# Kernel optimization log

Hardware: AMD Instinct MI355X
Metric: run time of the kernel (lower is better)

## Reference

```python
import jax, jax.numpy as jnp
import numpy as np

H = 128      # hidden_dim
HEADS = 4
HD = H // HEADS
B, S, D, A, I = 64, 512, 64, 3, 13


def layernorm(x, g, b, eps=1e-5):
    m = x.mean(-1, keepdims=True)
    v = ((x - m) ** 2).mean(-1, keepdims=True)
    return g * (x - m) / jnp.sqrt(v + eps) + b


def setup_inputs() -> dict:
    key = jax.random.key(0)
    ks = jax.random.split(key, 12)
    rn = lambda k, shp, s=0.05: jax.random.normal(k, shp, jnp.float32) * s
    return {
        "x": jax.random.normal(ks[0], (B, S, D), jnp.float32),
        "info": jax.random.normal(ks[1], (B, I), jnp.float32),
        "W_cell": rn(ks[2], (4 * H, D + H)), "b_cell": jnp.zeros(4 * H, jnp.float32),
        "Wqkv": rn(ks[3], (3 * H, H)), "bqkv": jnp.zeros(3 * H, jnp.float32),
        "Wo": rn(ks[4], (H, H)), "bo": jnp.zeros(H, jnp.float32),
        "ln_g": jnp.ones(H, jnp.float32), "ln_b": jnp.zeros(H, jnp.float32),
        "Wa1": rn(ks[5], (128, H + I)), "ba1": jnp.zeros(128, jnp.float32),
        "lna_g": jnp.ones(128, jnp.float32), "lna_b": jnp.zeros(128, jnp.float32),
        "Wa2": rn(ks[6], (A, 128)), "ba2": jnp.zeros(A, jnp.float32),
        "Wc1": rn(ks[7], (128, H + I)), "bc1": jnp.zeros(128, jnp.float32),
        "lnc_g": jnp.ones(128, jnp.float32), "lnc_b": jnp.zeros(128, jnp.float32),
        "Wc2": rn(ks[8], (1, 128)), "bc2": jnp.zeros(1, jnp.float32),
    }


def reference(x, info, W_cell, b_cell, Wqkv, bqkv, Wo, bo, ln_g, ln_b,
              Wa1, ba1, lna_g, lna_b, Wa2, ba2, Wc1, bc1, lnc_g, lnc_b, Wc2, bc2):
    Bx, Sx, _ = x.shape
    h0 = jnp.zeros((Bx, H), x.dtype)
    c0 = jnp.zeros((Bx, H), x.dtype)
    n0 = jnp.ones((Bx, H), x.dtype)

    def step(carry, xt):
        h, c, n = carry
        gates = jnp.concatenate([xt, h], -1) @ W_cell.T + b_cell
        i, f, o, z = jnp.split(gates, 4, axis=-1)
        i = jnp.exp(jnp.clip(i, -5.0, 5.0))
        f = jnp.exp(jnp.clip(f, -5.0, 5.0))
        c = jnp.clip(f * c + i * jnp.tanh(z), -1e6, 1e6)
        n = jnp.clip(f * n + i, 1e-6, 1e6)
        h = jnp.nan_to_num(jax.nn.sigmoid(o) * (c / n), nan=0.0, posinf=0.0, neginf=0.0)
        return (h, c, n), h

    _, hs = jax.lax.scan(step, (h0, c0, n0), jnp.swapaxes(x, 0, 1))  # (S,B,H)
    seq_h = jnp.swapaxes(hs, 0, 1)  # (B,S,H)

    # MultiheadAttention (self-attn, batch_first, shared in_proj)
    qkv = seq_h @ Wqkv.T + bqkv
    q, k, v = jnp.split(qkv, 3, -1)
    split_heads = lambda t: t.reshape(Bx, Sx, HEADS, HD).transpose(0, 2, 1, 3)
    q, k, v = split_heads(q), split_heads(k), split_heads(v)
    scores = jnp.einsum('bhqd,bhkd->bhqk', q, k) / np.sqrt(HD).astype(np.float32)
    attn = jax.nn.softmax(scores, axis=-1)
    av = jnp.einsum('bhqk,bhkd->bhqd', attn, v).transpose(0, 2, 1, 3).reshape(Bx, Sx, H)
    attn_out = av @ Wo.T + bo
    context = layernorm(seq_h + attn_out, ln_g, ln_b).mean(axis=1)  # (B,H)

    comb = jnp.concatenate([context, info], -1)  # (B, H+I)
    action_probs = jax.nn.softmax(
        jax.nn.relu(layernorm(comb @ Wa1.T + ba1, lna_g, lna_b)) @ Wa2.T + ba2, axis=-1)
    value = jax.nn.relu(layernorm(comb @ Wc1.T + bc1, lnc_g, lnc_b)) @ Wc2.T + bc2
    return (action_probs, value)
```

## Files before the change

kernel.cpp:

```cpp
#include <hip/hip_runtime.h>

typedef unsigned short ushort_t;
typedef unsigned int uint_t;

__device__ __forceinline__ float bflo(uint_t u){ union{uint_t i;float f;}v; v.i=u<<16; return v.f; }
__device__ __forceinline__ float bfhi(uint_t u){ union{uint_t i;float f;}v; v.i=u&0xffff0000u; return v.f; }
__device__ __forceinline__ float bfu(ushort_t u){ union{uint_t i;float f;}v; v.i=((uint_t)u)<<16; return v.f; }
__device__ __forceinline__ ushort_t f2b(float f){
  union{float f;uint_t i;}v; v.f=f;
  uint_t r = v.i + 0x7fffu + ((v.i>>16)&1u);
  return (ushort_t)(r>>16);
}
__device__ __forceinline__ void ld8bf(const ushort_t* p, float* w){
  uint4 u = *(const uint4*)p;
  w[0]=bflo(u.x); w[1]=bfhi(u.x); w[2]=bflo(u.y); w[3]=bfhi(u.y);
  w[4]=bflo(u.z); w[5]=bfhi(u.z); w[6]=bflo(u.w); w[7]=bfhi(u.w);
}
__device__ __forceinline__ void cvt8(uint4 u, float* d){
  d[0]=bflo(u.x); d[1]=bfhi(u.x); d[2]=bflo(u.y); d[3]=bfhi(u.y);
  d[4]=bflo(u.z); d[5]=bfhi(u.z); d[6]=bflo(u.w); d[7]=bfhi(u.w);
}
__device__ __forceinline__ float ldin(const void* p, size_t i, int isbf){
  return isbf ? bfu(((const ushort_t*)p)[i]) : ((const float*)p)[i];
}
__device__ __forceinline__ float rlane(float v, int l){
  return __uint_as_float(__builtin_amdgcn_readlane(__float_as_uint(v), l));
}

#define DOT128(acc, Wv, Bv) { float s0_=0.f,s1_=0.f,s2_=0.f,s3_=0.f; \
  _Pragma("unroll") \
  for (int k_=0;k_<128;k_+=4){ float4 h4_ = *(const float4*)&(Bv)[k_]; \
    s0_ += (Wv)[k_]*h4_.x; s1_ += (Wv)[k_+1]*h4_.y; \
    s2_ += (Wv)[k_+2]*h4_.z; s3_ += (Wv)[k_+3]*h4_.w; } \
  acc += (s0_+s1_)+(s2_+s3_); }
#define DOT64A(acc, Wv, Bv) { float s0_=0.f,s1_=0.f,s2_=0.f,s3_=0.f; \
  _Pragma("unroll") \
  for (int k_=0;k_<64;k_+=4){ float4 h4_ = *(const float4*)&(Bv)[k_]; \
    s0_ += (Wv)[k_]*h4_.x; s1_ += (Wv)[k_+1]*h4_.y; \
    s2_ += (Wv)[k_+2]*h4_.z; s3_ += (Wv)[k_+3]*h4_.w; } \
  acc += (s0_+s1_)+(s2_+s3_); }

typedef __attribute__((ext_vector_type(8))) short bf16x8;
typedef __attribute__((ext_vector_type(8))) _Float16 f16x8;
typedef __attribute__((ext_vector_type(4))) float f32x4;
__device__ __forceinline__ bf16x8 bcast8(uint4 u){ return __builtin_bit_cast(bf16x8, u); }
__device__ __forceinline__ f16x8  hcast8(uint4 u){ return __builtin_bit_cast(f16x8, u); }
__device__ __forceinline__ bf16x8 cvt8bf(const float* p){
  float4 a = *(const float4*)p; float4 b = *(const float4*)(p+4);
  uint4 u;
  u.x = (uint_t)f2b(a.x) | ((uint_t)f2b(a.y)<<16);
  u.y = (uint_t)f2b(a.z) | ((uint_t)f2b(a.w)<<16);
  u.z = (uint_t)f2b(b.x) | ((uint_t)f2b(b.y)<<16);
  u.w = (uint_t)f2b(b.z) | ((uint_t)f2b(b.w)<<16);
  return bcast8(u);
}
__device__ __forceinline__ void cvt8hl(const float* p, bf16x8* hi, bf16x8* lo){
  float v[8];
  *(float4*)&v[0] = *(const float4*)p;
  *(float4*)&v[4] = *(const float4*)(p+4);
  ushort_t h[8], l[8];
  #pragma unroll
  for (int j=0;j<8;++j){ h[j] = f2b(v[j]); l[j] = f2b(v[j] - bfu(h[j])); }
  uint4 uh = { (uint_t)h[0]|((uint_t)h[1]<<16), (uint_t)h[2]|((uint_t)h[3]<<16),
               (uint_t)h[4]|((uint_t)h[5]<<16), (uint_t)h[6]|((uint_t)h[7]<<16) };
  uint4 ul = { (uint_t)l[0]|((uint_t)l[1]<<16), (uint_t)l[2]|((uint_t)l[3]<<16),
               (uint_t)l[4]|((uint_t)l[5]<<16), (uint_t)l[6]|((uint_t)l[7]<<16) };
  *hi = bcast8(uh); *lo = bcast8(ul);
}
__device__ __forceinline__ ushort_t f2h(float f){
  _Float16 h = (_Float16)f;
  return __builtin_bit_cast(ushort_t, h);
}
__device__ __forceinline__ float h2f(ushort_t u){
  _Float16 h = __builtin_bit_cast(_Float16, u);
  return (float)h;
}

__global__ void k_detect(const uint_t* __restrict__ lng_raw, int* __restrict__ flag){
  if (threadIdx.x == 0) *flag = (lng_raw[0] == 0x3F803F80u) ? 1 : 0;
}

__global__ __launch_bounds__(256) void k_cvtw(const float* __restrict__ Wq,
    const float* __restrict__ Wo, const float* __restrict__ Wc,
    ushort_t* __restrict__ wqb, ushort_t* __restrict__ wob,
    ushort_t* __restrict__ wxh, ushort_t* __restrict__ wxl,
    ushort_t* __restrict__ whf, ushort_t* __restrict__ whl,
    const int* __restrict__ flag){
  if (*flag == 1) return;
  int i = blockIdx.x*256 + threadIdx.x;
  if (i < 12288){
    float4 f = ((const float4*)Wq)[i];
    uint2 u = { (uint_t)f2b(f.x) | ((uint_t)f2b(f.y)<<16),
                (uint_t)f2b(f.z) | ((uint_t)f2b(f.w)<<16) };
    ((uint2*)wqb)[i] = u;
  } else if (i < 16384){
    int k = i - 12288;
    float4 f = ((const float4*)Wo)[k];
    uint2 u = { (uint_t)f2b(f.x) | ((uint_t)f2b(f.y)<<16),
                (uint_t)f2b(f.z) | ((uint_t)f2b(f.w)<<16) };
    ((uint2*)wob)[k] = u;
  } else if (i < 24576){
    int k = i - 16384;
    int j = k >> 4, kq = (k & 15)*4;
    float4 f = *(const float4*)(Wc + (size_t)j*192 + kq);
    ushort_t h0=f2b(f.x), h1=f2b(f.y), h2=f2b(f.z), h3=f2b(f.w);
    ushort_t l0=f2b(f.x-bfu(h0)), l1=f2b(f.y-bfu(h1));
    ushort_t l2=f2b(f.z-bfu(h2)), l3=f2b(f.w-bfu(h3));
    ((uint2*)(wxh + (size_t)j*64 + kq))[0] = { (uint_t)h0|((uint_t)h1<<16), (uint_t)h2|((uint_t)h3<<16) };
    ((uint2*)(wxl + (size_t)j*64 + kq))[0] = { (uint_t)l0|((uint_t)l1<<16), (uint_t)l2|((uint_t)l3<<16) };
  } else if (i < 32768){
    int k2 = i - 24576;
    int jp = k2 >> 4, kc = (k2 & 15)*8;
    int wvp = jp >> 6, g = (jp >> 4) & 3, l = jp & 15;
    int jorig = 128*g + 16*wvp + l;
    const float* src = Wc + (size_t)jorig*192 + 64 + kc;
    ushort_t hh[8], ll[8];
    #pragma unroll
    for (int q=0;q<8;++q){
      hh[q] = f2h(src[q]);
      ll[q] = f2h(src[q] - h2f(hh[q]));
    }
    uint4 uh = { (uint_t)hh[0]|((uint_t)hh[1]<<16), (uint_t)hh[2]|((uint_t)hh[3]<<16),
                 (uint_t)hh[4]|((uint_t)hh[5]<<16), (uint_t)hh[6]|((uint_t)hh[7]<<16) };
    uint4 ul = { (uint_t)ll[0]|((uint_t)ll[1]<<16), (uint_t)ll[2]|((uint_t)ll[3]<<16),
                 (uint_t)ll[4]|((uint_t)ll[5]<<16), (uint_t)ll[6]|((uint_t)ll[7]<<16) };
    *(uint4*)(whf + (size_t)jp*136 + kc) = uh;
    *(uint4*)(whl + (size_t)jp*128 + kc) = ul;
  }
}

__global__ __launch_bounds__(256) void k_gx_bf(const void* __restrict__ x,
    const void* __restrict__ Wc, const void* __restrict__ bc,
    float* __restrict__ gx, const int* __restrict__ flag){
  if (*flag == 0) return;
  __shared__ float xs[2048];
  int row0 = blockIdx.x*32, t = threadIdx.x;
  {
    uint4 u = ((const uint4*)((const ushort_t*)x + (size_t)row0*64))[t];
    cvt8(u, &xs[t*8]);
  }
  __syncthreads();
  for (int pass=0; pass<2; ++pass){
    int j = t + pass*256;
    float w[64];
    const ushort_t* wr = (const ushort_t*)Wc + (size_t)j*192;
    #pragma unroll
    for (int q=0;q<8;q++) ld8bf(wr + 8*q, &w[8*q]);
    float bj = bfu(((const ushort_t*)bc)[j]);
    for (int s=0;s<32;++s){
      float acc = bj;
      DOT64A(acc, w, &xs[s*64]);
      gx[(size_t)(row0+s)*512 + j] = acc;
    }
  }
}

__global__ __launch_bounds__(256) void k_gx_f32(const float* __restrict__ x,
    const float* __restrict__ bc,
    const ushort_t* __restrict__ wxh, const ushort_t* __restrict__ wxl,
    float* __restrict__ gx, const int* __restrict__ flag){
  if (*flag == 1) return;
  int t = threadIdx.x, lane = t & 63, wave = t >> 6;
  int l16 = lane & 15, quad = lane >> 4;
  int rowb = blockIdx.x*64 + wave*16;
  const float* xp = x + (size_t)(rowb + l16)*64;
  bf16x8 xh0, xl0, xh1, xl1;
  cvt8hl(xp + quad*8,      &xh0, &xl0);
  cvt8hl(xp + 32 + quad*8, &xh1, &xl1);
  int r0 = rowb + quad*4;
  for (int ct=0; ct<32; ++ct){
    int j = ct*16 + l16;
    const ushort_t* bh = wxh + (size_t)j*64 + quad*8;
    const ushort_t* bl = wxl + (size_t)j*64 + quad*8;
    bf16x8 wh0 = bcast8(*(const uint4*)(bh));
    bf16x8 wh1 = bcast8(*(const uint4*)(bh + 32));
    bf16x8 wl0 = bcast8(*(const uint4*)(bl));
    bf16x8 wl1 = bcast8(*(const uint4*)(bl + 32));
    f32x4 acc = {0.f,0.f,0.f,0.f};
    acc = __builtin_amdgcn_mfma_f32_16x16x32_bf16(xh0, wh0, acc, 0,0,0);
    acc = __builtin_amdgcn_mfma_f32_16x16x32_bf16(xh1, wh1, acc, 0,0,0);
    acc = __builtin_amdgcn_mfma_f32_16x16x32_bf16(xh0, wl0, acc, 0,0,0);
    acc = __builtin_amdgcn_mfma_f32_16x16x32_bf16(xh1, wl1, acc, 0,0,0);
    acc = __builtin_amdgcn_mfma_f32_16x16x32_bf16(xl0, wh0, acc, 0,0,0);
    acc = __builtin_amdgcn_mfma_f32_16x16x32_bf16(xl1, wh1, acc, 0,0,0);
    float bj = bc[j];
    #pragma unroll
    for (int r=0;r<4;++r)
      gx[(size_t)(r0+r)*512 + j] = acc[r] + bj;
  }
}

__global__ __attribute__((amdgpu_flat_work_group_size(512,512), amdgpu_waves_per_eu(2,2)))
void k_rec_hl(const ushort_t* __restrict__ whf,
    const ushort_t* __restrict__ whl,
    const float* __restrict__ gx, float* __restrict__ seq_h,
    const int* __restrict__ flag){
  if (*flag == 1) return;
  int b = blockIdx.x, t = threadIdx.x;
  int lane = t & 63, wv = t >> 6, l16 = lane & 15, quad = lane >> 4;
  __shared__ ushort_t wlds[512*136];
  __shared__ ushort_t hz[2][448];
  {
    const uint4* src = (const uint4*)whf;
    uint4* dst = (uint4*)wlds;
    for (int i=t; i<8704; i+=512) dst[i] = src[i];
  }
  if (t < 448){ hz[0][t] = (ushort_t)0; hz[1][t] = (ushort_t)0; }
  const float* gxb = gx + (size_t)b*512*512;
  const int hidx = 16*wv + l16;
  float g0=0.f,g1=0.f,g2=0.f,g3=0.f;
  float c = 0.f, n = 1.f;
  if (quad == 0){
    g0 = gxb[hidx]; g1 = gxb[128+hidx]; g2 = gxb[256+hidx]; g3 = gxb[384+hidx];
  }
  float* shout = seq_h + (size_t)b*512*128;
  __syncthreads();
  const int c0 = 4*wv, c1 = 4*wv+1, c2 = 4*wv+2, c3 = 4*wv+3;
  const ushort_t* w0 = wlds + (c0*16 + l16)*136 + quad*8;
  const ushort_t* w1 = wlds + (c1*16 + l16)*136 + quad*8;
  const ushort_t* w2 = wlds + (c2*16 + l16)*136 + quad*8;
  const ushort_t* w3 = wlds + (c3*16 + l16)*136 + quad*8;
  const ushort_t* p0 = whl + (size_t)(c0*16 + l16)*128 + quad*8;
  const ushort_t* p1 = whl + (size_t)(c1*16 + l16)*128 + quad*8;
  const ushort_t* p2 = whl + (size_t)(c2*16 + l16)*128 + quad*8;
  const ushort_t* p3 = whl + (size_t)(c3*16 + l16)*128 + quad*8;
#define BDECL(T, ptr) uint4 T##0 = *(const uint4*)(ptr), T##1 = *(const uint4*)((ptr)+32), \
  T##2 = *(const uint4*)((ptr)+64), T##3 = *(const uint4*)((ptr)+96);
  BDECL(U0, w0) BDECL(U1, w1) BDECL(U2, w2) BDECL(U3, w3)
  BDECL(V0, p0) BDECL(V1, p1) BDECL(V2, p2) BDECL(V3, p3)
#undef BDECL
#define UPIN(U) asm volatile("" : "+v"(U.x), "+v"(U.y), "+v"(U.z), "+v"(U.w));
  UPIN(U00) UPIN(U01) UPIN(U02) UPIN(U03)
  UPIN(U10) UPIN(U11) UPIN(U12) UPIN(U13)
  UPIN(U20) UPIN(U21) UPIN(U22) UPIN(U23)
  UPIN(U30) UPIN(U31) UPIN(U32) UPIN(U33)
  UPIN(V00) UPIN(V01) UPIN(V02) UPIN(V03)
  UPIN(V10) UPIN(V11) UPIN(V12) UPIN(V13)
  UPIN(V20) UPIN(V21) UPIN(V22) UPIN(V23)
  UPIN(V30) UPIN(V31) UPIN(V32) UPIN(V33)
#undef UPIN
  const int hoff = ((l16 == 0) ? 0 : ((l16 == 1) ? 160 : 320)) + quad*8;
  const ushort_t* hzA = hz[0] + hoff;
  const ushort_t* hzB = hz[1] + hoff;
  for (int ts=0; ts<512; ++ts){
    const ushort_t* src = (ts & 1) ? hzB : hzA;
    ushort_t* dstbuf = (ts & 1) ? hz[0] : hz[1];
    f16x8 A0 = hcast8(*(const uint4*)(src));
    f16x8 A1 = hcast8(*(const uint4*)(src + 32));
    f16x8 A2 = hcast8(*(const uint4*)(src + 64));
    f16x8 A3 = hcast8(*(const uint4*)(src + 96));
    f32x4 s0 = {0.f,0.f,0.f,0.f}, s1 = {0.f,0.f,0.f,0.f};
    f32x4 s2 = {0.f,0.f,0.f,0.f}, s3 = {0.f,0.f,0.f,0.f};
#define TILE(sa, Uf, Vf) \
    sa = __builtin_amdgcn_mfma_f32_16x16x32_f16(A0, hcast8(Uf##0), sa, 0,0,0); \
    sa = __builtin_amdgcn_mfma_f32_16x16x32_f16(A1, hcast8(Uf##1), sa, 0,0,0); \
    sa = __builtin_amdgcn_mfma_f32_16x16x32_f16(A2, hcast8(Uf##2), sa, 0,0,0); \
    sa = __builtin_amdgcn_mfma_f32_16x16x32_f16(A3, hcast8(Uf##3), sa, 0,0,0); \
    sa = __builtin_amdgcn_mfma_f32_16x16x32_f16(A0, hcast8(Vf##0), sa, 0,0,0); \
    sa = __builtin_amdgcn_mfma_f32_16x16x32_f16(A1, hcast8(Vf##1), sa, 0,0,0); \
    sa = __builtin_amdgcn_mfma_f32_16x16x32_f16(A2, hcast8(Vf##2), sa, 0,0,0); \
    sa = __builtin_amdgcn_mfma_f32_16x16x32_f16(A3, hcast8(Vf##3), sa, 0,0,0);
    TILE(s0, U0, V0)
    TILE(s1, U1, V1)
    TILE(s2, U2, V2)
    TILE(s3, U3, V3)
#undef TILE
    if (quad == 0){
      float gi = s0[0] + s0[1] + g0;
      float gf = s1[0] + s1[1] + g1;
      float go = s2[0] + s2[1] + g2;
      float gz = s3[0] + s3[1] + g3;
      if (ts+1 < 512){
        const float* gn = gxb + (size_t)(ts+1)*512;
        g0 = gn[hidx]; g1 = gn[128+hidx]; g2 = gn[256+hidx]; g3 = gn[384+hidx];
      }
      float ii = __expf(fminf(fmaxf(gi,-5.f),5.f));
      float ff = __expf(fminf(fmaxf(gf,-5.f),5.f));
      float e2 = __expf(2.f*gz);
      float zt = 1.f - 2.f/(e2+1.f);
      c = fminf(fmaxf(ff*c + ii*zt, -1e6f), 1e6f);
      n = fminf(fmaxf(ff*n + ii, 1e-6f), 1e6f);
      float oo = 1.f/(1.f+__expf(-go));
      float h = oo*(c/n);
      if (!isfinite(h)) h = 0.f;
      shout[(size_t)ts*128 + hidx] = h;
      ushort_t hhi = f2h(h);
      dstbuf[hidx] = hhi;
      dstbuf[160 + hidx] = f2h(h - h2f(hhi));
    }
    __syncthreads();
  }
}

__global__ __launch_bounds__(1024, 4) void k_rec_bf(const void* __restrict__ Wc,
    const float* __restrict__ gx, float* __restrict__ seq_h,
    const int* __restrict__ flag){
  if (*flag == 0) return;
  int b = blockIdx.x, t = threadIdx.x;
  int lane = t & 63, j = t & 511, half = t >> 9;
  __shared__ float ps[1024];
  __shared__ float hs[128];
  uint_t wu[32];
  {
    const uint4* wp = (const uint4*)((const ushort_t*)Wc + (size_t)j*192 + 64 + 64*half);
    #pragma unroll
    for (int q=0;q<8;q++){ uint4 u = wp[q];
      wu[4*q]=u.x; wu[4*q+1]=u.y; wu[4*q+2]=u.z; wu[4*q+3]=u.w; }
  }
  const float* gxb = gx + (size_t)b*512*512;
  float g0=0.f, g1=0.f;
  if (half==0){ g0 = gxb[j]; g1 = gxb[512 + j]; }
  float hreg = 0.f;
  float c = 0.f, n = 1.f;
  float* shout = seq_h + (size_t)b*512*128;
  for (int ts=0; ts<512; ++ts){
    float a0, a1=0.f, a2=0.f, a3=0.f;
    if (half==0){
      a0 = g0; g0 = g1;
      g1 = (ts+2 < 512) ? gxb[(size_t)(ts+2)*512 + j] : 0.f;
    } else a0 = 0.f;
    #pragma unroll
    for (int kk=0; kk<32; kk+=2){
      float h0v = rlane(hreg, 2*kk),   h1v = rlane(hreg, 2*kk+1);
      float h2v = rlane(hreg, 2*kk+2), h3v = rlane(hreg, 2*kk+3);
      a0 = fmaf(bflo(wu[kk]),   h0v, a0);
      a1 = fmaf(bfhi(wu[kk]),   h1v, a1);
      a2 = fmaf(bflo(wu[kk+1]), h2v, a2);
      a3 = fmaf(bfhi(wu[kk+1]), h3v, a3);
    }
    ps[t] = (a0+a1)+(a2+a3);
    __syncthreads();
    if (t < 128){
      float gi = ps[t]     + ps[512+t];
      float gf = ps[128+t] + ps[640+t];
      float go = ps[256+t] + ps[768+t];
      float gz = ps[384+t] + ps[896+t];
      float ii = __expf(fminf(fmaxf(gi,-5.f),5.f));
      float ff = __expf(fminf(fmaxf(gf,-5.f),5.f));
      float e2 = __expf(2.f*gz);
      float zt = 1.f - 2.f/(e2+1.f);
      c = fminf(fmaxf(ff*c + ii*zt, -1e6f), 1e6f);
      n = fminf(fmaxf(ff*n + ii, 1e-6f), 1e6f);
      float oo = 1.f/(1.f+__expf(-go));
      float h = oo*(c/n);
      if (!isfinite(h)) h = 0.f;
      hs[t] = h;
      shout[(size_t)ts*128 + t] = h;
    }
    __syncthreads();
    hreg = hs[(half<<6) | lane];
  }
}

__global__ __launch_bounds__(512) void k_rec_inl(const void* __restrict__ x,
    const void* __restrict__ Wc, const void* __restrict__ bc,
    float* __restrict__ seq_h, const int* __restrict__ flag){
  int isbf = *flag;
  int b = blockIdx.x, j = threadIdx.x;
  __shared__ float hs[128];
  __shared__ float gs[512];
  __shared__ float xr[4][64];
  float w[128], wx[64];
  if (isbf){
    const ushort_t* wr = (const ushort_t*)Wc + (size_t)j*192;
    #pragma unroll
    for (int q=0;q<8;q++)  ld8bf(wr + 8*q, &wx[8*q]);
    #pragma unroll
    for (int q=0;q<16;q++) ld8bf(wr + 64 + 8*q, &w[8*q]);
  } else {
    const float* wr = (const float*)Wc + (size_t)j*192;
    #pragma unroll
    for (int q=0;q<16;q++){ float4 f=*(const float4*)(wr+4*q);
      wx[4*q]=f.x; wx[4*q+1]=f.y; wx[4*q+2]=f.z; wx[4*q+3]=f.w; }
    #pragma unroll
    for (int q=0;q<32;q++){ float4 f=*(const float4*)(wr+64+4*q);
      w[4*q]=f.x; w[4*q+1]=f.y; w[4*q+2]=f.z; w[4*q+3]=f.w; }
  }
  float bj = ldin(bc, j, isbf);
  float c = 0.f, n = 1.f;
  if (j < 128) hs[j] = 0.f;
  if (j < 128){
    int r = j>>6, k = j&63;
    xr[r][k] = ldin(x, ((size_t)b*512 + r)*64 + k, isbf);
  }
  __syncthreads();
  for (int t=0; t<512; ++t){
    const float* xt = xr[t&3];
    float acc = bj;
    DOT64A(acc, wx, xt);
    DOT128(acc, w, hs);
    gs[j] = acc;
    __syncthreads();
    if (j < 128){
      float gi=gs[j], gf=gs[128+j], go=gs[256+j], gz=gs[384+j];
      float ii = __expf(fminf(fmaxf(gi,-5.f),5.f));
      float ff = __expf(fminf(fmaxf(gf,-5.f),5.f));
      float e2 = __expf(2.f*gz);
      float zt = 1.f - 2.f/(e2+1.f);
      c = fminf(fmaxf(ff*c + ii*zt, -1e6f), 1e6f);
      n = fminf(fmaxf(ff*n + ii, 1e-6f), 1e6f);
      float oo = 1.f/(1.f+__expf(-go));
      float h = oo*(c/n);
      if (!isfinite(h)) h = 0.f;
      hs[j] = h;
      seq_h[((size_t)b*512 + t)*128 + j] = h;
    } else if (j >= 448 && (t+2) < 512){
      int k = j & 63;
      xr[(t+2)&3][k] = ldin(x, ((size_t)b*512 + (t+2))*64 + k, isbf);
    }
    __syncthreads();
  }
}

__global__ __launch_bounds__(256) void k_qkv(const float* __restrict__ seq_h,
    const void* __restrict__ Wq, const void* __restrict__ bq,
    const ushort_t* __restrict__ wqb,
    ushort_t* __restrict__ qkv, const int* __restrict__ flag){
  int isbf = *flag;
  int row0 = blockIdx.x*32, t = threadIdx.x;
  if (isbf){
    __shared__ float hsb[4096];
    {
      const float4* hp = (const float4*)(seq_h + (size_t)row0*128);
      #pragma unroll
      for (int i=t;i<1024;i+=256) ((float4*)hsb)[i] = hp[i];
    }
    __syncthreads();
    for (int pass=0; pass<2; ++pass){
      int j = (pass==0) ? t : 256 + t;
      if (j >= 384) break;
      float w[128];
      const ushort_t* wr = (const ushort_t*)Wq + (size_t)j*128;
      #pragma unroll
      for (int q=0;q<16;q++) ld8bf(wr + 8*q, &w[8*q]);
      float bj = bfu(((const ushort_t*)bq)[j]);
      for (int s=0;s<32;++s){
        float acc = bj;
        DOT128(acc, w, &hsb[s*128]);
        qkv[(size_t)(row0+s)*384 + j] = f2b(acc);
      }
    }
  } else {
    int lane = t & 63, wave = t >> 6, l16 = lane & 15, quad = lane >> 4;
    int rt = wave & 1, chalf = wave >> 1;
    int rowg = row0 + rt*16 + l16;
    const float* hp = seq_h + (size_t)rowg*128 + quad*8;
    bf16x8 A0 = cvt8bf(hp);
    bf16x8 A1 = cvt8bf(hp + 32);
    bf16x8 A2 = cvt8bf(hp + 64);
    bf16x8 A3 = cvt8bf(hp + 96);
    int rbase = row0 + rt*16 + quad*4;
    for (int ci=0; ci<12; ++ci){
      int ct = chalf*12 + ci;
      int col = ct*16 + l16;
      const ushort_t* wb = wqb + (size_t)col*128 + quad*8;
      f32x4 acc = {0.f,0.f,0.f,0.f};
      acc = __builtin_amdgcn_mfma_f32_16x16x32_bf16(A0, bcast8(*(const uint4*)(wb)),      acc, 0,0,0);
      acc = __builtin_amdgcn_mfma_f32_16x16x32_bf16(A1, bcast8(*(const uint4*)(wb + 32)), acc, 0,0,0);
      acc = __builtin_amdgcn_mfma_f32_16x16x32_bf16(A2, bcast8(*(const uint4*)(wb + 64)), acc, 0,0,0);
      acc = __builtin_amdgcn_mfma_f32_16x16x32_bf16(A3, bcast8(*(const uint4*)(wb + 96)), acc, 0,0,0);
      float bj = ((const float*)bq)[col];
      #pragma unroll
      for (int r=0;r<4;++r)
        qkv[(size_t)(rbase+r)*384 + col] = f2b(acc[r] + bj);
    }
  }
}

#define AROW4(OP) OP(0) OP(1) OP(2) OP(3)
__global__ __launch_bounds__(512) void k_attn(const ushort_t* __restrict__ qkv,
    ushort_t* __restrict__ av){
  int b = blockIdx.x >> 2, h = blockIdx.x & 3;
  int t = threadIdx.x, lane = t & 63, wave = t >> 6;
  int l16 = lane & 15, quad = lane >> 4;
  __shared__ ushort_t Vt[32*512];
  __shared__ ushort_t Pl[8*16*64];
  const ushort_t* base = qkv + (size_t)b*512*384 + h*32;
  {
    const ushort_t* vr = base + (size_t)t*384 + 256;
    ushort_t tmp[32];
    *(uint4*)&tmp[0]  = *(const uint4*)(vr);
    *(uint4*)&tmp[8]  = *(const uint4*)(vr+8);
    *(uint4*)&tmp[16] = *(const uint4*)(vr+16);
    *(uint4*)&tmp[24] = *(const uint4*)(vr+24);
    #pragma unroll
    for (int d=0; d<32; ++d) Vt[d*512 + t] = tmp[d];
  }
  __syncthreads();
  ushort_t* Pw = Pl + wave*16*64;
  const float scale = 0.17677669529663687f;
  for (int q4=0; q4<4; ++q4){
    int qt = wave + q4*8;
    bf16x8 qa;
    { uint4 u = *(const uint4*)(base + (size_t)(qt*16 + l16)*384 + quad*8);
      qa = bcast8(u); }
    f32x4 O0 = {0.f,0.f,0.f,0.f}, O1 = {0.f,0.f,0.f,0.f};
    float m0=-1e30f,m1=-1e30f,m2=-1e30f,m3=-1e30f;
    float l0=0.f,l1=0.f,l2=0.f,l3=0.f;
    for (int ch=0; ch<8; ++ch){
      f32x4 S0,S1,S2,S3;
      {
        const ushort_t* kb = base + 128 + quad*8;
        uint4 u0 = *(const uint4*)(kb + (size_t)(ch*64 +  0 + l16)*384);
        uint4 u1 = *(const uint4*)(kb + (size_t)(ch*64 + 16 + l16)*384);
        uint4 u2 = *(const uint4*)(kb + (size_t)(ch*64 + 32 + l16)*384);
        uint4 u3 = *(const uint4*)(kb + (size_t)(ch*64 + 48 + l16)*384);
        f32x4 z = {0.f,0.f,0.f,0.f};
        S0 = __builtin_amdgcn_mfma_f32_16x16x32_bf16(qa, bcast8(u0), z, 0,0,0);
        S1 = __builtin_amdgcn_mfma_f32_16x16x32_bf16(qa, bcast8(u1), z, 0,0,0);
        S2 = __builtin_amdgcn_mfma_f32_16x16x32_bf16(qa, bcast8(u2), z, 0,0,0);
        S3 = __builtin_amdgcn_mfma_f32_16x16x32_bf16(qa, bcast8(u3), z, 0,0,0);
      }
#define CMAX(r) float c##r = fmaxf(fmaxf(S0[r],S1[r]), fmaxf(S2[r],S3[r])) * scale; \
      c##r = fmaxf(c##r, __shfl_xor(c##r,1)); c##r = fmaxf(c##r, __shfl_xor(c##r,2)); \
      c##r = fmaxf(c##r, __shfl_xor(c##r,4)); c##r = fmaxf(c##r, __shfl_xor(c##r,8)); \
      float M##r = fmaxf(m##r, c##r); float al##r = __expf(m##r - M##r); \
      m##r = M##r; O0[r] *= al##r; O1[r] *= al##r; l##r *= al##r;
      AROW4(CMAX)
#undef CMAX
#define PEXP(r) float ps##r; { \
      float p0 = __expf(S0[r]*scale - m##r); \
      float p1 = __expf(S1[r]*scale - m##r); \
      float p2 = __expf(S2[r]*scale - m##r); \
      float p3 = __expf(S3[r]*scale - m##r); \
      ps##r = (p0+p1)+(p2+p3); \
      Pw[(quad*4+(r))*64 +  0 + l16] = f2b(p0); \
      Pw[(quad*4+(r))*64 + 16 + l16] = f2b(p1); \
      Pw[(quad*4+(r))*64 + 32 + l16] = f2b(p2); \
      Pw[(quad*4+(r))*64 + 48 + l16] = f2b(p3); }
      AROW4(PEXP)
#undef PEXP
#define PSUM(r) ps##r += __shfl_xor(ps##r,1); ps##r += __shfl_xor(ps##r,2); \
      ps##r += __shfl_xor(ps##r,4); ps##r += __shfl_xor(ps##r,8); l##r += ps##r;
      AROW4(PSUM)
#undef PSUM
      asm volatile("s_waitcnt lgkmcnt(0)" ::: "memory");
      bf16x8 pa0, pa1;
      { uint4 u = *(const uint4*)&Pw[l16*64 + quad*8];      pa0 = bcast8(u); }
      { uint4 u = *(const uint4*)&Pw[l16*64 + 32 + quad*8]; pa1 = bcast8(u); }
      {
        uint4 v0 = *(const uint4*)&Vt[(l16)*512    + ch*64 + quad*8];
        uint4 v1 = *(const uint4*)&Vt[(l16)*512    + ch*64 + 32 + quad*8];
        uint4 v2 = *(const uint4*)&Vt[(16+l16)*512 + ch*64 + quad*8];
        uint4 v3 = *(const uint4*)&Vt[(16+l16)*512 + ch*64 + 32 + quad*8];
        O0 = __builtin_amdgcn_mfma_f32_16x16x32_bf16(pa0, bcast8(v0), O0, 0,0,0);
        O0 = __builtin_amdgcn_mfma_f32_16x16x32_bf16(pa1, bcast8(v1), O0, 0,0,0);
        O1 = __builtin_amdgcn_mfma_f32_16x16x32_bf16(pa0, bcast8(v2), O1, 0,0,0);
        O1 = __builtin_amdgcn_mfma_f32_16x16x32_bf16(pa1, bcast8(v3), O1, 0,0,0);
      }
    }
#define OST(r) { float iv = 1.f/l##r; int row = qt*16 + quad*4 + (r); \
      ushort_t* op = av + (size_t)(b*512 + row)*128 + h*32; \
      op[l16]      = f2b(O0[r]*iv); \
      op[16 + l16] = f2b(O1[r]*iv); }
    AROW4(OST)
#undef OST
  }
}

__global__ __launch_bounds__(256) void k_ctx(const ushort_t* __restrict__ av,
    const float* __restrict__ seq_h, const void* __restrict__ Wo,
    const void* __restrict__ bo_, const void* __restrict__ lng,
    const void* __restrict__ lnb, const ushort_t* __restrict__ wob,
    float* __restrict__ partial, const int* __restrict__ flag){
  int isbf = *flag;
  __shared__ float rs[4096];
  __shared__ float mrow[32], srow[32];
  __shared__ float halfsum[128];
  int row0 = blockIdx.x*32, t = threadIdx.x;
  int j = t & 127, sh = t >> 7;
  if (isbf){
    __shared__ float avs[4096];
    {
      const uint4* ap = (const uint4*)(av + (size_t)row0*128);
      for (int i=t;i<512;i+=256) cvt8(ap[i], &avs[i*8]);
    }
    __syncthreads();
    float w[128];
    const ushort_t* wr = (const ushort_t*)Wo + (size_t)j*128;
    #pragma unroll
    for (int q=0;q<16;q++) ld8bf(wr + 8*q, &w[8*q]);
    float bj = bfu(((const ushort_t*)bo_)[j]);
    for (int si=0; si<16; ++si){
      int s = sh*16 + si;
      float acc = bj;
      DOT128(acc, w, &avs[s*128]);
      rs[s*128+j] = acc + seq_h[(size_t)(row0+s)*128 + j];
    }
  } else {
    int lane = t & 63, wave = t >> 6, l16 = lane & 15, quad = lane >> 4;
    int rt = wave & 1, chalf = wave >> 1;
    int rowg = row0 + rt*16 + l16;
    const ushort_t* ap = av + (size_t)rowg*128 + quad*8;
    bf16x8 A0 = bcast8(*(const uint4*)(ap));
    bf16x8 A1 = bcast8(*(const uint4*)(ap + 32));
    bf16x8 A2 = bcast8(*(const uint4*)(ap + 64));
    bf16x8 A3 = bcast8(*(const uint4*)(ap + 96));
    int rl0 = rt*16 + quad*4;
    for (int ci=0; ci<4; ++ci){
      int ct = chalf*4 + ci;
      int col = ct*16 + l16;
      const ushort_t* wb = wob + (size_t)col*128 + quad*8;
      f32x4 acc = {0.f,0.f,0.f,0.f};
      acc = __builtin_amdgcn_mfma_f32_16x16x32_bf16(A0, bcast8(*(const uint4*)(wb)),      acc, 0,0,0);
      acc = __builtin_amdgcn_mfma_f32_16x16x32_bf16(A1, bcast8(*(const uint4*)(wb + 32)), acc, 0,0,0);
      acc = __builtin_amdgcn_mfma_f32_16x16x32_bf16(A2, bcast8(*(const uint4*)(wb + 64)), acc, 0,0,0);
      acc = __builtin_amdgcn_mfma_f32_16x16x32_bf16(A3, bcast8(*(const uint4*)(wb + 96)), acc, 0,0,0);
      float bj2 = ((const float*)bo_)[col];
      #pragma unroll
      for (int r=0;r<4;++r){
        int rl = rl0 + r;
        rs[rl*128 + col] = acc[r] + bj2 + seq_h[(size_t)(row0+rl)*128 + col];
      }
    }
  }
  __syncthreads();
  {
    int rr = t>>3, part = t&7;
    float vals[16], sm = 0.f;
    #pragma unroll
    for (int k2=0;k2<16;k2++){ vals[k2] = rs[rr*128 + part + 8*k2]; sm += vals[k2]; }
    sm += __shfl_xor(sm,1); sm += __shfl_xor(sm,2); sm += __shfl_xor(sm,4);
    float mean = sm*(1.f/128.f);
    float vv = 0.f;
    #pragma unroll
    for (int k2=0;k2<16;k2++){ float d = vals[k2]-mean; vv += d*d; }
    vv += __shfl_xor(vv,1); vv += __shfl_xor(vv,2); vv += __shfl_xor(vv,4);
    if (part==0){ mrow[rr]=mean; srow[rr]=rsqrtf(vv*(1.f/128.f)+1e-5f); }
  }
  __syncthreads();
  float g = ldin(lng, j, isbf), bb = ldin(lnb, j, isbf);
  float accs = 0.f;
  for (int si=0; si<16; ++si){
    int s = sh*16 + si;
    accs += g*(rs[s*128+j]-mrow[s])*srow[s] + bb;
  }
  if (sh==0) halfsum[j] = accs;
  __syncthreads();
  if (sh==1){
    int bidx = row0>>9, tile = (row0>>5)&15;
    partial[((size_t)bidx*16 + tile)*128 + j] = halfsum[j] + accs;
  }
}

__global__ __launch_bounds__(128) void k_head(const float* __restrict__ partial,
    const void* __restrict__ info,
    const void* Wa1, const void* ba1, const void* lnag, const void* lnab,
    const void* Wa2, const void* ba2,
    const void* Wc1, const void* bc1, const void* lncg, const void* lncb,
    const void* Wc2, const void* bc2, void* __restrict__ out,
    const int* __restrict__ flag){
  int isbf = *flag;
  int b = blockIdx.x, t = threadIdx.x;
  __shared__ float comb[144];
  __shared__ float red[128];
  __shared__ float uu[128];
  float s = 0.f;
  #pragma unroll
  for (int i=0;i<16;i++) s += partial[((size_t)b*16+i)*128 + t];
  comb[t] = s*(1.f/512.f);
  if (t < 13) comb[128+t] = ldin(info, (size_t)b*13+t, isbf);
  __syncthreads();
  for (int br=0; br<2; ++br){
    const void* W1 = br ? Wc1 : Wa1;
    const void* b1 = br ? bc1 : ba1;
    const void* lg_ = br ? lncg : lnag;
    const void* lb_ = br ? lncb : lnab;
    float a = ldin(b1, t, isbf);
    for (int k=0;k<141;k++) a += ldin(W1, (size_t)t*141+k, isbf)*comb[k];
    red[t] = a; __syncthreads();
    for (int st=64; st>0; st>>=1){ if (t<st) red[t]+=red[t+st]; __syncthreads(); }
    float mean = red[0]*(1.f/128.f);
    __syncthreads();
    float d = a - mean;
    red[t] = d*d; __syncthreads();
    for (int st=64; st>0; st>>=1){ if (t<st) red[t]+=red[t+st]; __syncthreads(); }
    float rstd = rsqrtf(red[0]*(1.f/128.f)+1e-5f);
    __syncthreads();
    float u = ldin(lg_, t, isbf)*d*rstd + ldin(lb_, t, isbf);
    uu[t] = fmaxf(u, 0.f);
    __syncthreads();
    if (br==0){
      if (t < 3){
        float lg2 = ldin(ba2, t, isbf);
        for (int k=0;k<128;k++) lg2 += ldin(Wa2, (size_t)t*128+k, isbf)*uu[k];
        red[t] = lg2;
      }
      __syncthreads();
      if (t==0){
        float mx = fmaxf(red[0], fmaxf(red[1], red[2]));
        float e0=__expf(red[0]-mx), e1=__expf(red[1]-mx), e2=__expf(red[2]-mx);
        float inv = 1.f/(e0+e1+e2);
        if (isbf){
          ushort_t* o = (ushort_t*)out;
          o[b*3+0]=f2b(e0*inv); o[b*3+1]=f2b(e1*inv); o[b*3+2]=f2b(e2*inv);
        } else {
          float* o = (float*)out;
          o[b*3+0]=e0*inv; o[b*3+1]=e1*inv; o[b*3+2]=e2*inv;
        }
      }
      __syncthreads();
    } else {
      if (t==0){
        float v = ldin(bc2, 0, isbf);
        for (int k=0;k<128;k++) v += ldin(Wc2, k, isbf)*uu[k];
        if (isbf) ((ushort_t*)out)[192 + b] = f2b(v);
        else      ((float*)out)[192 + b] = v;
      }
    }
  }
}

extern "C" void kernel_launch(void* const* d_in, const int* in_sizes, int n_in,
                              void* d_out, int out_size, void* d_ws, size_t ws_size,
                              hipStream_t stream){
  const void* x    = d_in[0];
  const void* info = d_in[1];
  const void* Wcell= d_in[2];
  const void* bcell= d_in[3];
  const void* Wqkv = d_in[4];
  const void* bqkv = d_in[5];
  const void* Wo   = d_in[6];
  const void* bo   = d_in[7];
  const void* lng  = d_in[8];
  const void* lnb  = d_in[9];
  const void* Wa1  = d_in[10];
  const void* ba1  = d_in[11];
  const void* lnag = d_in[12];
  const void* lnab = d_in[13];
  const void* Wa2  = d_in[14];
  const void* ba2  = d_in[15];
  const void* Wc1  = d_in[16];
  const void* bc1  = d_in[17];
  const void* lncg = d_in[18];
  const void* lncb = d_in[19];
  const void* Wc2  = d_in[20];
  const void* bc2  = d_in[21];

  char* ws = (char*)d_ws;
  const int bigws = (ws_size >= ((size_t)82<<20)) ? 1 : 0;
  float*    seqh = (float*)   ws;
  float*    gxf  = (float*)   (ws + ((size_t)16<<20));
  ushort_t* qkv  = (ushort_t*)(ws + ((size_t)16<<20));
  ushort_t* av   = (ushort_t*)(ws + ((size_t)40<<20));
  float*    part = (float*)   (ws + ((size_t)48<<20));
  int*      flag = bigws ? (int*)(ws + ((size_t)80<<20))
                         : (int*)(ws + ((size_t)48<<20) + (512<<10));
  ushort_t* wqb  = (ushort_t*)(ws + ((size_t)80<<20) + (1<<20));
  ushort_t* wob  = wqb + 384*128;
  ushort_t* wxh  = wob + 128*128;
  ushort_t* wxl  = wxh + 512*64;
  ushort_t* whf  = wxl + 512*64;
  ushort_t* whl  = whf + 512*136;

  k_detect<<<1, 64, 0, stream>>>((const uint_t*)lng, flag);
  if (bigws){
    k_cvtw  <<< 128, 256, 0, stream>>>((const float*)Wqkv, (const float*)Wo,
                                       (const float*)Wcell, wqb, wob, wxh, wxl, whf, whl, flag);
    k_gx_bf <<<1024, 256, 0, stream>>>(x, Wcell, bcell, gxf, flag);
    k_gx_f32<<< 512, 256, 0, stream>>>((const float*)x, (const float*)bcell,
                                       wxh, wxl, gxf, flag);
    k_rec_bf <<< 64, 1024, 0, stream>>>(Wcell, gxf, seqh, flag);
    k_rec_hl <<< 64,  512, 0, stream>>>(whf, whl, gxf, seqh, flag);
  } else {
    k_rec_inl<<<64, 512, 0, stream>>>(x, Wcell, bcell, seqh, flag);
    k_cvtw  <<< 128, 256, 0, stream>>>((const float*)Wqkv, (const float*)Wo,
                                       (const float*)Wcell, wqb, wob, wxh, wxl, whf, whl, flag);
  }
  k_qkv <<<1024, 256, 0, stream>>>(seqh, Wqkv, bqkv, wqb, qkv, flag);
  k_attn<<< 256, 512, 0, stream>>>(qkv, av);
  k_ctx <<<1024, 256, 0, stream>>>(av, seqh, Wo, bo, lng, lnb, wob, part, flag);
  k_head<<<  64, 128, 0, stream>>>(part, info, Wa1, ba1, lnag, lnab, Wa2, ba2,
                                   Wc1, bc1, lncg, lncb, Wc2, bc2, d_out, flag);
}
```

Measured before the change: 698.2 us.

## Interleave gate layout, prefetch gates four steps ahead, use LDS-only barrier

The input-projection kernel now writes the four gate values of each hidden unit next to each other, so the recurrent kernel can fetch all four with one float4 load. The recurrent loop is unrolled by four, with four rotating float4 registers that prefetch gate inputs four timesteps ahead. __syncthreads is replaced by an explicit lgkmcnt wait plus s_barrier, so the barrier no longer waits for outstanding global loads and the seq_h stores. This is meant to take global-memory latency off the serial 512-step critical path. The risk is that any other reader of gx that still expects the old layout would now get wrong values.

Result: no change. 691.6 us (-1.0%).

```diff
diff --git a/kernel.cpp b/kernel.cpp
--- a/kernel.cpp
+++ b/kernel.cpp
@@ -184,9 +184,10 @@
     acc = __builtin_amdgcn_mfma_f32_16x16x32_bf16(xl0, wh0, acc, 0,0,0);
     acc = __builtin_amdgcn_mfma_f32_16x16x32_bf16(xl1, wh1, acc, 0,0,0);
     float bj = bc[j];
+    int dcol = ((j & 127) << 2) + (j >> 7);
     #pragma unroll
     for (int r=0;r<4;++r)
-      gx[(size_t)(r0+r)*512 + j] = acc[r] + bj;
+      gx[(size_t)(r0+r)*512 + dcol] = acc[r] + bj;
   }
 }
 
@@ -208,10 +209,14 @@
   if (t < 448){ hz[0][t] = (ushort_t)0; hz[1][t] = (ushort_t)0; }
   const float* gxb = gx + (size_t)b*512*512;
   const int hidx = 16*wv + l16;
-  float g0=0.f,g1=0.f,g2=0.f,g3=0.f;
   float c = 0.f, n = 1.f;
+  const float* gxp = gxb + ((size_t)hidx << 2);
+  float4 P0 = {0.f,0.f,0.f,0.f}, P1 = P0, P2 = P0, P3 = P0;
   if (quad == 0){
-    g0 = gxb[hidx]; g1 = gxb[128+hidx]; g2 = gxb[256+hidx]; g3 = gxb[384+hidx];
+    P0 = *(const float4*)(gxp);
+    P1 = *(const float4*)(gxp + 512);
+    P2 = *(const float4*)(gxp + 1024);
+    P3 = *(const float4*)(gxp + 1536);
   }
   float* shout = seq_h + (size_t)b*512*128;
   __syncthreads();
@@ -242,15 +247,6 @@
   const int hoff = ((l16 == 0) ? 0 : ((l16 == 1) ? 160 : 320)) + quad*8;
   const ushort_t* hzA = hz[0] + hoff;
   const ushort_t* hzB = hz[1] + hoff;
-  for (int ts=0; ts<512; ++ts){
-    const ushort_t* src = (ts & 1) ? hzB : hzA;
-    ushort_t* dstbuf = (ts & 1) ? hz[0] : hz[1];
-    f16x8 A0 = hcast8(*(const uint4*)(src));
-    f16x8 A1 = hcast8(*(const uint4*)(src + 32));
-    f16x8 A2 = hcast8(*(const uint4*)(src + 64));
-    f16x8 A3 = hcast8(*(const uint4*)(src + 96));
-    f32x4 s0 = {0.f,0.f,0.f,0.f}, s1 = {0.f,0.f,0.f,0.f};
-    f32x4 s2 = {0.f,0.f,0.f,0.f}, s3 = {0.f,0.f,0.f,0.f};
 #define TILE(sa, Uf, Vf) \
     sa = __builtin_amdgcn_mfma_f32_16x16x32_f16(A0, hcast8(Uf##0), sa, 0,0,0); \
     sa = __builtin_amdgcn_mfma_f32_16x16x32_f16(A1, hcast8(Uf##1), sa, 0,0,0); \
@@ -260,36 +256,54 @@
     sa = __builtin_amdgcn_mfma_f32_16x16x32_f16(A1, hcast8(Vf##1), sa, 0,0,0); \
     sa = __builtin_amdgcn_mfma_f32_16x16x32_f16(A2, hcast8(Vf##2), sa, 0,0,0); \
     sa = __builtin_amdgcn_mfma_f32_16x16x32_f16(A3, hcast8(Vf##3), sa, 0,0,0);
-    TILE(s0, U0, V0)
-    TILE(s1, U1, V1)
-    TILE(s2, U2, V2)
-    TILE(s3, U3, V3)
+#define STEPBODY(TS, PAR, PS) { \
+    const ushort_t* asrc = (PAR) ? hzB : hzA; \
+    ushort_t* dstbuf = (PAR) ? hz[0] : hz[1]; \
+    f16x8 A0 = hcast8(*(const uint4*)(asrc)); \
+    f16x8 A1 = hcast8(*(const uint4*)(asrc + 32)); \
+    f16x8 A2 = hcast8(*(const uint4*)(asrc + 64)); \
+    f16x8 A3 = hcast8(*(const uint4*)(asrc + 96)); \
+    f32x4 s0 = {0.f,0.f,0.f,0.f}, s1 = {0.f,0.f,0.f,0.f}; \
+    f32x4 s2 = {0.f,0.f,0.f,0.f}, s3 = {0.f,0.f,0.f,0.f}; \
+    TILE(s0, U0, V0) \
+    TILE(s1, U1, V1) \
+    TILE(s2, U2, V2) \
+    TILE(s3, U3, V3) \
+    if (quad == 0){ \
+       \
+      float gi = s0[0] + s0[1] + PS.x; \
+      float gf = s1[0] + s1[1] + PS.y; \
+      float go = s2[0] + s2[1] + PS.z; \
+      float gz = s3[0] + s3[1] + PS.w; \
+      { int nts_ = (TS) + 4; if (nts_ >= 512) nts_ = 0;         \
+        PS = *(const float4*)(gxp + (size_t)nts_*512); }        \
+      float ii = __expf(fminf(fmaxf(gi,-5.f),5.f)); \
+      float ff = __expf(fminf(fmaxf(gf,-5.f),5.f)); \
+      float e2 = __expf(2.f*gz); \
+      float zt = 1.f - 2.f/(e2+1.f); \
+      c = fminf(fmaxf(ff*c + ii*zt, -1e6f), 1e6f); \
+      n = fminf(fmaxf(ff*n + ii, 1e-6f), 1e6f); \
+      float oo = 1.f/(1.f+__expf(-go)); \
+      float h = oo*(c/n); \
+      if (!isfinite(h)) h = 0.f; \
+      shout[(size_t)(TS)*128 + hidx] = h; \
+      ushort_t hhi = f2h(h); \
+      dstbuf[hidx] = hhi; \
+      dstbuf[160 + hidx] = f2h(h - h2f(hhi)); \
+    } \
+     \
+    asm volatile("s_waitcnt lgkmcnt(0)" ::: "memory"); \
+    __builtin_amdgcn_s_barrier(); \
+    asm volatile("" ::: "memory"); \
+  }
+  for (int ts=0; ts<512; ts+=4){
+    STEPBODY(ts,   0, P0)
+    STEPBODY(ts+1, 1, P1)
+    STEPBODY(ts+2, 0, P2)
+    STEPBODY(ts+3, 1, P3)
+  }
+#undef STEPBODY
 #undef TILE
-    if (quad == 0){
-      float gi = s0[0] + s0[1] + g0;
-      float gf = s1[0] + s1[1] + g1;
-      float go = s2[0] + s2[1] + g2;
-      float gz = s3[0] + s3[1] + g3;
-      if (ts+1 < 512){
-        const float* gn = gxb + (size_t)(ts+1)*512;
-        g0 = gn[hidx]; g1 = gn[128+hidx]; g2 = gn[256+hidx]; g3 = gn[384+hidx];
-      }
-      float ii = __expf(fminf(fmaxf(gi,-5.f),5.f));
-      float ff = __expf(fminf(fmaxf(gf,-5.f),5.f));
-      float e2 = __expf(2.f*gz);
-      float zt = 1.f - 2.f/(e2+1.f);
-      c = fminf(fmaxf(ff*c + ii*zt, -1e6f), 1e6f);
-      n = fminf(fmaxf(ff*n + ii, 1e-6f), 1e6f);
-      float oo = 1.f/(1.f+__expf(-go));
-      float h = oo*(c/n);
-      if (!isfinite(h)) h = 0.f;
-      shout[(size_t)ts*128 + hidx] = h;
-      ushort_t hhi = f2h(h);
-      dstbuf[hidx] = hhi;
-      dstbuf[160 + hidx] = f2h(h - h2f(hhi));
-    }
-    __syncthreads();
-  }
 }
 
 __global__ __launch_bounds__(1024, 4) void k_rec_bf(const void* __restrict__ Wc,
```
